# Performance work log

Hardware: AMD Instinct MI355X
Metric: run time of the kernel (lower is better)

The kernel has to match this reference:

```python
import jax, jax.numpy as jnp
import numpy as np

V = 32000       # word vocab size
K = 24          # max n-grams per word (n=3, word len <= 9 -> 3*len-3 <= 24)
NG = 200000     # n_gram_size (hash table size)
E = 128         # emb_size
B, S = 16, 2048 # batch, seq_len


def setup_inputs() -> dict:
    key = jax.random.key(0)
    k1, k2, k3, k4 = jax.random.split(key, 4)
    word_idx = jax.random.randint(k1, (B, S), 0, V, dtype=jnp.int32)
    # hashed n-gram ids live in [4, NG), matching _hash(word) % (NG-4) + 4
    ngram_ids = jax.random.randint(k2, (V, K), 4, NG, dtype=jnp.int32)
    ngram_counts = jax.random.randint(k3, (V,), 1, K + 1, dtype=jnp.int32)
    # pad unused slots with id 0 (padding_idx -> zero embedding row)
    pos = jnp.arange(K)[None, :]
    ngram_ids = jnp.where(pos < ngram_counts[:, None], ngram_ids, 0)
    # special tokens (<4): direct lookup of their own embedding row, count 1
    sp = jnp.arange(4)
    ngram_ids = ngram_ids.at[sp, :].set(0).at[sp, 0].set(sp)
    ngram_counts = ngram_counts.at[sp].set(1)
    emb_table = jax.random.normal(k4, (NG, E), dtype=jnp.float32)
    return {"word_idx": word_idx, "ngram_ids": ngram_ids,
            "ngram_counts": ngram_counts, "emb_table": emb_table}


def reference(word_idx, ngram_ids, ngram_counts, emb_table):
    # nn.Embedding(padding_idx=0): row 0 is zero
    table = emb_table.at[0].set(0.0)
    g = ngram_ids[word_idx]                 # [B, S, K] gathered n-gram ids
    e = table[g]                            # [B, S, K, E] gathered embeddings
    cnt = ngram_counts[word_idx].astype(e.dtype)[..., None]  # [B, S, 1]
    # padded slots point at the zero row, so a plain sum == masked sum
    return e.sum(axis=2) / cnt              # [B, S, E] mean over n-grams
```

## Files before the change

kernel.cpp:

```cpp
#include <hip/hip_runtime.h>

#define NUM_WORDS 32768
#define KMAX 24
#define GROUP 8

__global__ __launch_bounds__(256) void ngram_emb_kernel(
    const int* __restrict__ word_idx,
    const int* __restrict__ ngram_ids,
    const int* __restrict__ ngram_counts,
    const float* __restrict__ emb_table,
    float* __restrict__ out)
{
    const int gtid = blockIdx.x * blockDim.x + threadIdx.x;
    const int word = gtid >> 6;
    const int lane = threadIdx.x & 63;

    const int w   = __builtin_amdgcn_readfirstlane(word_idx[word]);
    const int cnt = ngram_counts[w];
    const int* ids = ngram_ids + w * KMAX;

    int rr[KMAX];
#pragma unroll
    for (int k = 0; k < KMAX; ++k)
        rr[k] = __builtin_amdgcn_readfirstlane(ids[k]);

    const float2* tbl = (const float2*)emb_table;
    float ax = 0.f, ay = 0.f;

#pragma unroll
    for (int g = 0; g < KMAX; g += GROUP) {
        if (g < cnt) {
            float2 v[GROUP];
            float  m[GROUP];
#pragma unroll
            for (int j = 0; j < GROUP; ++j) {
                const int r = rr[g + j];
                m[j] = r ? 1.f : 0.f;
                v[j] = tbl[(long)r * 64 + lane];
            }
#pragma unroll
            for (int j = 0; j < GROUP; ++j) {
                ax = fmaf(m[j], v[j].x, ax);
                ay = fmaf(m[j], v[j].y, ay);
            }
        }
    }

    const float inv = 1.0f / (float)cnt;
    float2 o; o.x = ax * inv; o.y = ay * inv;
    ((float2*)out)[(long)word * 64 + lane] = o;
}

extern "C" void kernel_launch(void* const* d_in, const int* in_sizes, int n_in,
                              void* d_out, int out_size, void* d_ws, size_t ws_size,
                              hipStream_t stream) {
    const int*   word_idx     = (const int*)d_in[0];
    const int*   ngram_ids    = (const int*)d_in[1];
    const int*   ngram_counts = (const int*)d_in[2];
    const float* emb_table    = (const float*)d_in[3];
    float*       out          = (float*)d_out;

    const int threads = 256;
    const int blocks  = (NUM_WORDS * 64) / threads;
    ngram_emb_kernel<<<blocks, threads, 0, stream>>>(
        word_idx, ngram_ids, ngram_counts, emb_table, out);
}
```

Before: 169.5 us.

## Split each wave into two halves gathering alternate n-gram rows with float4 loads

Each 64-lane wave now covers two n-gram rows per load instruction: the lower half reads even-indexed rows and the upper half odd rows, each lane fetching a float4 of a 128-float row. A two-buffer issue/consume schedule keeps the next group of loads in flight while the previous group is accumulated, and the halves are combined with a cross-half shuffle. The output is written by half the lanes with a nontemporal store, and launch bounds request higher occupancy. The goal is fewer, wider memory instructions and more loads in flight per wave, at the cost of an extra shuffle reduction and idle lanes during the store.

```diff
diff --git a/kernel.cpp b/kernel.cpp
--- a/kernel.cpp
+++ b/kernel.cpp
@@ -2,9 +2,10 @@
 
 #define NUM_WORDS 32768
 #define KMAX 24
-#define GROUP 8
 
-__global__ __launch_bounds__(256) void ngram_emb_kernel(
+typedef float f4 __attribute__((ext_vector_type(4)));
+
+__global__ __launch_bounds__(256, 8) void ngram_emb_kernel(
     const int* __restrict__ word_idx,
     const int* __restrict__ ngram_ids,
     const int* __restrict__ ngram_counts,
@@ -14,9 +15,11 @@
     const int gtid = blockIdx.x * blockDim.x + threadIdx.x;
     const int word = gtid >> 6;
     const int lane = threadIdx.x & 63;
+    const int half = lane >> 5;
+    const int col  = lane & 31;
 
     const int w   = __builtin_amdgcn_readfirstlane(word_idx[word]);
-    const int cnt = ngram_counts[w];
+    const int cnt = __builtin_amdgcn_readfirstlane(ngram_counts[w]);
     const int* ids = ngram_ids + w * KMAX;
 
     int rr[KMAX];
@@ -24,31 +27,44 @@
     for (int k = 0; k < KMAX; ++k)
         rr[k] = __builtin_amdgcn_readfirstlane(ids[k]);
 
-    const float2* tbl = (const float2*)emb_table;
-    float ax = 0.f, ay = 0.f;
+    const f4* tbl = (const f4*)emb_table;
 
-#pragma unroll
-    for (int g = 0; g < KMAX; g += GROUP) {
-        if (g < cnt) {
-            float2 v[GROUP];
-            float  m[GROUP];
-#pragma unroll
-            for (int j = 0; j < GROUP; ++j) {
-                const int r = rr[g + j];
-                m[j] = r ? 1.f : 0.f;
-                v[j] = tbl[(long)r * 64 + lane];
-            }
-#pragma unroll
-            for (int j = 0; j < GROUP; ++j) {
-                ax = fmaf(m[j], v[j].x, ax);
-                ay = fmaf(m[j], v[j].y, ay);
-            }
-        }
+    f4    v[8];
+    float m[8];
+    f4    acc = (f4){0.f, 0.f, 0.f, 0.f};
+
+#define ISSUE(G, BUF)                                               \
+    _Pragma("unroll")                                               \
+    for (int j = 0; j < 4; ++j) {                                   \
+        const int re = rr[(G)*8 + 2*j];                             \
+        const int ro = rr[(G)*8 + 2*j + 1];                         \
+        const int r  = half ? ro : re;      \
+        m[(BUF) + j] = (r != 0) ? 1.f : 0.f;                        \
+        v[(BUF) + j] = tbl[(long)r * 32 + col];                     \
     }
 
-    const float inv = 1.0f / (float)cnt;
-    float2 o; o.x = ax * inv; o.y = ay * inv;
-    ((float2*)out)[(long)word * 64 + lane] = o;
+#define CONSUME(BUF)                                                \
+    _Pragma("unroll")                                               \
+    for (int j = 0; j < 4; ++j)                                     \
+        acc += m[(BUF) + j] * v[(BUF) + j];
+
+    ISSUE(0, 0);
+    if (cnt > 8)  { ISSUE(1, 4); }
+    CONSUME(0);
+    if (cnt > 16) { ISSUE(2, 0); }
+    if (cnt > 8)  { CONSUME(4); }
+    if (cnt > 16) { CONSUME(0); }
+
+    acc.x += __shfl_xor(acc.x, 32);
+    acc.y += __shfl_xor(acc.y, 32);
+    acc.z += __shfl_xor(acc.z, 32);
+    acc.w += __shfl_xor(acc.w, 32);
+
+    if (half == 0) {
+        const float inv = 1.0f / (float)cnt;
+        f4 o = acc * inv;
+        __builtin_nontemporal_store(o, (f4*)out + (long)word * 32 + col);
+    }
 }
 
 extern "C" void kernel_launch(void* const* d_in, const int* in_sizes, int n_in,
```

Measured after the change: 225.4 us. 1.33x slower.
